# Optimization experiments

Measured on AMD Instinct MI355X. Metric: run time of the kernel, lower is better.

## Reference

```python
import jax, jax.numpy as jnp
import numpy as np

N, C_IN, C_OUT, H = 4096, 1024, 512, 4
D = C_OUT // H  # per-head output dim
TEMP = 1.0


def setup_inputs() -> dict:
    key = jax.random.key(0)
    ks = jax.random.split(key, 6)
    node_feats = jax.random.normal(ks[0], (N, C_IN), dtype=jnp.float32)
    # sparse 0/1 adjacency mask, avg degree ~ 0.02*N
    adj_matrix = jax.random.bernoulli(ks[1], 0.02, (N, N)).astype(jnp.float32)
    lim_w = np.sqrt(6.0 / (C_IN + D))
    lim_v = np.sqrt(6.0 / (D + 1))
    W = jax.random.uniform(ks[2], (H, C_IN, D), jnp.float32, -lim_w, lim_w)
    b = jnp.zeros((H, D), dtype=jnp.float32)
    v0 = jax.random.uniform(ks[3], (H, D), jnp.float32, -lim_v, lim_v)
    v1 = jax.random.uniform(ks[4], (H, D), jnp.float32, -lim_v, lim_v)
    return {"node_feats": node_feats, "adj_matrix": adj_matrix,
            "W": W, "b": b, "v0": v0, "v1": v1}


def reference(node_feats, adj_matrix, W, b, v0, v1):
    # per-head linear projection: [H, N, D]
    h = jnp.einsum('nc,hcd->hnd', node_feats, W) + b[:, None, :]
    f1 = jnp.einsum('hnd,hd->hn', h, v0)  # [H, N]
    f2 = jnp.einsum('hnd,hd->hn', h, v1)  # [H, N]
    logits = adj_matrix[None, :, :] * (f1[:, :, None] + f2[:, None, :])
    # torch to_sparse drops exact zeros; sparse.softmax normalizes over
    # the remaining (nonzero) entries only, zeros stay zero when densified.
    mask = logits != 0
    vals = (jax.nn.sigmoid(logits) - 0.5) / TEMP
    rowmax = jnp.max(jnp.where(mask, vals, -1e30), axis=-1, keepdims=True)
    e = jnp.where(mask, jnp.exp(vals - rowmax), 0.0)
    denom = jnp.sum(e, axis=-1, keepdims=True)
    p = jnp.where(denom > 0, e / jnp.maximum(denom, 1e-30), 0.0)
    out = jnp.einsum('hnm,hmd->hnd', p, h)  # [H, N, D]
    # concat heads along feature dim -> [N, H*D]
    return out.transpose(1, 0, 2).reshape(node_feats.shape[0], -1)
```

## Files before the change

### kernel.cpp

```cpp
#include <hip/hip_runtime.h>
#include <hip/hip_bf16.h>

#define N_NODES 4096
#define C_IN    1024
#define H_HEADS 4
#define D_HEAD  128
#define C_OUT   512
#define DEG_CAP 256

typedef __attribute__((ext_vector_type(8))) short short8;
typedef __attribute__((ext_vector_type(8))) unsigned short u16x8;
typedef __attribute__((ext_vector_type(4))) float f32x4;

__device__ __forceinline__ unsigned short f2bf(float f) {
    unsigned u = __float_as_uint(f);
    u += 0x7FFFu + ((u >> 16) & 1u);
    return (unsigned short)(u >> 16);
}
__device__ __forceinline__ float bf2f(unsigned short u) {
    return __uint_as_float((unsigned)u << 16);
}
__device__ __forceinline__ float sigv(float s) {
    return 1.f / (1.f + __expf(-s)) - 0.5f;
}

#define GLOAD_LDS16(gp, lp)                                                        \
    __builtin_amdgcn_global_load_lds(                                              \
        (const __attribute__((address_space(1))) unsigned int*)(gp),               \
        (__attribute__((address_space(3))) unsigned int*)(lp), 16, 0, 0)

__global__ void k_cvt(const float* __restrict__ X, const float* __restrict__ W,
                      unsigned short* __restrict__ Xb, unsigned short* __restrict__ Wt,
                      float* __restrict__ F12) {
    if (blockIdx.x < 2048) {
        int g = blockIdx.x * blockDim.x + threadIdx.x;
        const float4* s = (const float4*)(X + (size_t)g * 8);
        float4 a = s[0], b = s[1];
        ushort4 p0, p1;
        p0.x = f2bf(a.x); p0.y = f2bf(a.y); p0.z = f2bf(a.z); p0.w = f2bf(a.w);
        p1.x = f2bf(b.x); p1.y = f2bf(b.y); p1.z = f2bf(b.z); p1.w = f2bf(b.w);
        ushort4* d = (ushort4*)(Xb + (size_t)g * 8);
        d[0] = p0; d[1] = p1;
    } else if (blockIdx.x < 2560) {
        int g = (blockIdx.x - 2048) * blockDim.x + threadIdx.x;
        int o = g * 4;
        int c  = o & 1023;
        int hd = o >> 10;
        int d  = hd & 127;
        int h  = hd >> 7;
        const float* src = W + (size_t)h * C_IN * D_HEAD + (size_t)c * D_HEAD + d;
        ushort4 p;
        p.x = f2bf(src[0 * D_HEAD]);
        p.y = f2bf(src[1 * D_HEAD]);
        p.z = f2bf(src[2 * D_HEAD]);
        p.w = f2bf(src[3 * D_HEAD]);
        *(ushort4*)(Wt + o) = p;
    } else {
        int g = (blockIdx.x - 2560) * blockDim.x + threadIdx.x;
        *(f32x4*)(F12 + (size_t)g * 4) = (f32x4){0.f, 0.f, 0.f, 0.f};
    }
}

__global__ void k_work(const unsigned short* __restrict__ Xb,
                       const unsigned short* __restrict__ Wt,
                       const float* __restrict__ bias,
                       const float* __restrict__ v0, const float* __restrict__ v1,
                       const float* __restrict__ adj,
                       unsigned short* __restrict__ Hb,
                       float* __restrict__ F1, float* __restrict__ F2,
                       unsigned short* __restrict__ idx, int* __restrict__ nnz) {
    __shared__ __align__(16) unsigned char smem[32768];
    const int t    = threadIdx.x;
    const int lane = t & 63;
    const int wid  = t >> 6;

    if (blockIdx.x < 512) {
        unsigned short* ldsA = (unsigned short*)smem;
        unsigned short* ldsB = ldsA + 2 * 64 * 64;
        const int wrow = wid >> 1, wcol = wid & 1;
        const int bid  = blockIdx.x;
        const int lin  = (bid & 7) * 64 + (bid >> 3);
        const int rowStart = (lin >> 3) * 64;
        const int colStart = (lin & 7) * 64;

        f32x4 acc[2][2];
#pragma unroll
        for (int m = 0; m < 2; ++m)
#pragma unroll
            for (int n = 0; n < 2; ++n) acc[m][n] = (f32x4){0.f, 0.f, 0.f, 0.f};

        const int lrow = lane >> 2;
        const int lkq  = (lane & 3) ^ ((lane >> 3) & 3);

        auto stage = [&](int buf, int k0) {
#pragma unroll
            for (int ii = 0; ii < 2; ++ii) {
                int c  = wid * 2 + ii;
                int h  = c >> 2, rb = c & 3;
                const unsigned short* g =
                    Xb + (size_t)(rowStart + rb * 16 + lrow) * C_IN + k0 + h * 32 + lkq * 8;
                GLOAD_LDS16(g, ldsA + buf * 4096 + h * 2048 + rb * 512);
            }
#pragma unroll
            for (int ii = 0; ii < 2; ++ii) {
                int c  = wid * 2 + ii;
                int h  = c >> 2, db = c & 3;
                const unsigned short* g =
                    Wt + (size_t)(colStart + db * 16 + lrow) * C_IN + k0 + h * 32 + lkq * 8;
                GLOAD_LDS16(g, ldsB + buf * 4096 + h * 2048 + db * 512);
            }
        };

        stage(0, 0);
        __syncthreads();

        const int fr = lane & 15;
        const int sw = ((lane >> 4) ^ ((fr >> 1) & 3)) * 8;
        int cur = 0;
        for (int kt = 0; kt < 16; ++kt) {
            if (kt < 15) stage(cur ^ 1, (kt + 1) * 64);
            const unsigned short* __restrict__ lA = ldsA + cur * 4096;
            const unsigned short* __restrict__ lB = ldsB + cur * 4096;
#pragma unroll
            for (int h = 0; h < 2; ++h) {
                short8 bfr[2];
#pragma unroll
                for (int n = 0; n < 2; ++n)
                    bfr[n] = *(const short8*)(lB + h * 2048 + (wcol * 32 + n * 16 + fr) * 32 + sw);
#pragma unroll
                for (int m = 0; m < 2; ++m) {
                    short8 a = *(const short8*)(lA + h * 2048 + (wrow * 32 + m * 16 + fr) * 32 + sw);
#pragma unroll
                    for (int n = 0; n < 2; ++n)
                        acc[m][n] = __builtin_amdgcn_mfma_f32_16x16x32_bf16(a, bfr[n], acc[m][n], 0, 0, 0);
                }
            }
            __syncthreads();
            cur ^= 1;
        }

        const int c0 = colStart + wcol * 32 + (lane & 15);
        const int c1 = c0 + 16;
        const int head = c0 >> 7;
        const float bb0 = bias[c0], bb1 = bias[c1];
        const float v0c0 = v0[c0], v0c1 = v0[c1];
        const float v1c0 = v1[c0], v1c1 = v1[c1];
#pragma unroll
        for (int m = 0; m < 2; ++m) {
            int row_g = rowStart + wrow * 32 + m * 16 + (lane >> 4) * 4;
#pragma unroll
            for (int r = 0; r < 4; ++r) {
                float h0 = acc[m][0][r] + bb0;
                float h1 = acc[m][1][r] + bb1;
                Hb[(size_t)(row_g + r) * C_OUT + c0] = f2bf(h0);
                Hb[(size_t)(row_g + r) * C_OUT + c1] = f2bf(h1);
                float p1 = h0 * v0c0 + h1 * v0c1;
                float p2 = h0 * v1c0 + h1 * v1c1;
#pragma unroll
                for (int off = 8; off; off >>= 1) {
                    p1 += __shfl_xor(p1, off);
                    p2 += __shfl_xor(p2, off);
                }
                if ((lane & 15) == 0) {
                    atomicAdd(&F1[(row_g + r) * 4 + head], p1);
                    atomicAdd(&F2[(row_g + r) * 4 + head], p2);
                }
            }
        }
    } else {
        int* wtot = (int*)smem;
        const int i = blockIdx.x - 512;
        const float4* arow = (const float4*)(adj + (size_t)i * N_NODES);
        float4 av[4];
#pragma unroll
        for (int r = 0; r < 4; ++r) av[r] = arow[r * 256 + t];

        int cnt = 0;
#pragma unroll
        for (int r = 0; r < 4; ++r)
            cnt += (av[r].x != 0.f) + (av[r].y != 0.f) + (av[r].z != 0.f) + (av[r].w != 0.f);
        int v = cnt;
#pragma unroll
        for (int off = 1; off < 64; off <<= 1) {
            int u = __shfl_up(v, off);
            if (lane >= off) v += u;
        }
        if (lane == 63) wtot[wid] = v;
        __syncthreads();
        int wpre = 0, total = 0;
#pragma unroll
        for (int w = 0; w < 4; ++w) {
            int tw = wtot[w];
            if (w < wid) wpre += tw;
            total += tw;
        }
        int off = wpre + v - cnt;
        unsigned short* ir = idx + (size_t)i * DEG_CAP;
#pragma unroll
        for (int r = 0; r < 4; ++r) {
            int j0 = (r * 256 + t) * 4;
            if (av[r].x != 0.f) { if (off < DEG_CAP) ir[off] = (unsigned short)j0;       off++; }
            if (av[r].y != 0.f) { if (off < DEG_CAP) ir[off] = (unsigned short)(j0 + 1); off++; }
            if (av[r].z != 0.f) { if (off < DEG_CAP) ir[off] = (unsigned short)(j0 + 2); off++; }
            if (av[r].w != 0.f) { if (off < DEG_CAP) ir[off] = (unsigned short)(j0 + 3); off++; }
        }
        if (t == 0) nnz[i] = min(total, DEG_CAP);
    }
}

__global__ void k_pv(const unsigned short* __restrict__ idx, const int* __restrict__ nnz,
                     const float* __restrict__ F1, const float* __restrict__ F2,
                     const unsigned short* __restrict__ Hb, float* __restrict__ Out) {
    __shared__ unsigned short jl[DEG_CAP];
    __shared__ float ev[H_HEADS][DEG_CAP];

    const int i    = blockIdx.x;
    const int t    = threadIdx.x;
    const int lane = t & 63;
    const int w    = t >> 6;

    const int nv = nnz[i];

    ushort4 jv = *(const ushort4*)(idx + (size_t)i * DEG_CAP + 4 * lane);
    *(ushort4*)(jl + 4 * lane) = jv;

    const float f1h = F1[i * 4 + w];
    float dsum = 0.f;
#pragma unroll
    for (int s = 0; s < 4; ++s) {
        int e = lane + 64 * s;
        float ee = 0.f;
        if (e < nv) {
            int j = jl[e];
            float sg = f1h + F2[j * 4 + w];
            ee = (sg != 0.f) ? __expf(sigv(sg)) : 0.f;
        }
        ev[w][e] = ee;
        dsum += ee;
    }
#pragma unroll
    for (int o2 = 32; o2; o2 >>= 1) dsum += __shfl_xor(dsum, o2);

    const unsigned short* __restrict__ hp = Hb + (size_t)w * D_HEAD + 2 * lane;
    float a0 = 0.f, a1 = 0.f, b0 = 0.f, b1 = 0.f;
    int jj = 0;
#pragma unroll 4
    for (; jj + 1 < nv; jj += 2) {
        int ja = jl[jj], jb = jl[jj + 1];
        float ea = ev[w][jj], eb = ev[w][jj + 1];
        unsigned pa = *(const unsigned*)(hp + (size_t)ja * C_OUT);
        unsigned pb = *(const unsigned*)(hp + (size_t)jb * C_OUT);
        a0 += ea * bf2f((unsigned short)(pa & 0xFFFFu));
        a1 += ea * bf2f((unsigned short)(pa >> 16));
        b0 += eb * bf2f((unsigned short)(pb & 0xFFFFu));
        b1 += eb * bf2f((unsigned short)(pb >> 16));
    }
    if (jj < nv) {
        int ja = jl[jj];
        float ea = ev[w][jj];
        unsigned pa = *(const unsigned*)(hp + (size_t)ja * C_OUT);
        a0 += ea * bf2f((unsigned short)(pa & 0xFFFFu));
        a1 += ea * bf2f((unsigned short)(pa >> 16));
    }

    float2 o;
    if (dsum > 0.f) {
        float inv = 1.f / fmaxf(dsum, 1e-30f);
        o.x = (a0 + b0) * inv;
        o.y = (a1 + b1) * inv;
    } else {
        o.x = 0.f; o.y = 0.f;
    }
    *(float2*)(Out + (size_t)i * C_OUT + w * D_HEAD + 2 * lane) = o;
}

extern "C" void kernel_launch(void* const* d_in, const int* in_sizes, int n_in,
                              void* d_out, int out_size, void* d_ws, size_t ws_size,
                              hipStream_t stream) {
    const float* X   = (const float*)d_in[0];
    const float* adj = (const float*)d_in[1];
    const float* W   = (const float*)d_in[2];
    const float* b   = (const float*)d_in[3];
    const float* v0  = (const float*)d_in[4];
    const float* v1  = (const float*)d_in[5];
    float* out = (float*)d_out;

    char* ws = (char*)d_ws;
    unsigned short* Wt  = (unsigned short*)ws;
    unsigned short* Xb  = (unsigned short*)(ws + (size_t)1 * 1024 * 1024);
    unsigned short* Hb  = (unsigned short*)(ws + (size_t)9 * 1024 * 1024);
    float*          F1  = (float*)(ws + (size_t)13 * 1024 * 1024);
    float*          F2  = F1 + N_NODES * 4;
    unsigned short* idx = (unsigned short*)(ws + (size_t)14 * 1024 * 1024);
    int*            nnz = (int*)(ws + (size_t)16 * 1024 * 1024);

    k_cvt<<<2592, 256, 0, stream>>>(X, W, Xb, Wt, F1);
    k_work<<<512 + N_NODES, 256, 0, stream>>>(Xb, Wt, b, v0, v1, adj, Hb, F1, F2, idx, nnz);
    k_pv<<<N_NODES, 256, 0, stream>>>(idx, nnz, F1, F2, Hb, out);
}
```

Before: 59.70 us.

## Move adjacency compaction into prep kernel, split GEMM out, widen gather loads

Adjacency row compaction now runs in the same launch as the bf16 conversion of X and W, and the GEMM becomes its own kernel with statically sized LDS. Conversion blocks now handle 32 elements of X per thread, and the F1/F2 zeroing is folded into the first 32 blocks. The PV gather now splits each wave into two halves, each lane loading 4 bf16 values per neighbour row, with a cross-half shuffle reduction at the end. The aim is to rebalance work across launches so the large adjacency scan no longer shares a launch with the GEMM, and to issue fewer, wider gather loads, at the cost of half the lanes sitting idle during the final store.

```diff
diff --git a/kernel.cpp b/kernel.cpp
--- a/kernel.cpp
+++ b/kernel.cpp
@@ -10,6 +10,7 @@
 
 typedef __attribute__((ext_vector_type(8))) short short8;
 typedef __attribute__((ext_vector_type(8))) unsigned short u16x8;
+typedef __attribute__((ext_vector_type(4))) unsigned short u16x4;
 typedef __attribute__((ext_vector_type(4))) float f32x4;
 
 __device__ __forceinline__ unsigned short f2bf(float f) {
@@ -29,146 +30,44 @@
         (const __attribute__((address_space(1))) unsigned int*)(gp),               \
         (__attribute__((address_space(3))) unsigned int*)(lp), 16, 0, 0)
 
-__global__ void k_cvt(const float* __restrict__ X, const float* __restrict__ W,
-                      unsigned short* __restrict__ Xb, unsigned short* __restrict__ Wt,
-                      float* __restrict__ F12) {
-    if (blockIdx.x < 2048) {
-        int g = blockIdx.x * blockDim.x + threadIdx.x;
-        const float4* s = (const float4*)(X + (size_t)g * 8);
-        float4 a = s[0], b = s[1];
-        ushort4 p0, p1;
-        p0.x = f2bf(a.x); p0.y = f2bf(a.y); p0.z = f2bf(a.z); p0.w = f2bf(a.w);
-        p1.x = f2bf(b.x); p1.y = f2bf(b.y); p1.z = f2bf(b.z); p1.w = f2bf(b.w);
-        ushort4* d = (ushort4*)(Xb + (size_t)g * 8);
-        d[0] = p0; d[1] = p1;
-    } else if (blockIdx.x < 2560) {
-        int g = (blockIdx.x - 2048) * blockDim.x + threadIdx.x;
-        int o = g * 4;
+__global__ void k_prep(const float* __restrict__ X, const float* __restrict__ W,
+                       const float* __restrict__ adj,
+                       unsigned short* __restrict__ Xb, unsigned short* __restrict__ Wt,
+                       float* __restrict__ F12,
+                       unsigned short* __restrict__ idx, int* __restrict__ nnz) {
+    __shared__ int wtot[4];
+    const int t    = threadIdx.x;
+    const int lane = t & 63;
+    const int wid  = t >> 6;
+
+    if (blockIdx.x < 512) {
+        size_t g = (size_t)blockIdx.x * 256 + t;
+        const float4* s = (const float4*)(X + g * 32);
+        ushort4* d = (ushort4*)(Xb + g * 32);
+#pragma unroll
+        for (int q = 0; q < 8; ++q) {
+            float4 a = s[q];
+            ushort4 p;
+            p.x = f2bf(a.x); p.y = f2bf(a.y); p.z = f2bf(a.z); p.w = f2bf(a.w);
+            d[q] = p;
+        }
+        int o = ((int)blockIdx.x * 256 + t) * 4;
         int c  = o & 1023;
         int hd = o >> 10;
-        int d  = hd & 127;
+        int dd = hd & 127;
         int h  = hd >> 7;
-        const float* src = W + (size_t)h * C_IN * D_HEAD + (size_t)c * D_HEAD + d;
+        const float* src = W + (size_t)h * C_IN * D_HEAD + (size_t)c * D_HEAD + dd;
         ushort4 p;
         p.x = f2bf(src[0 * D_HEAD]);
         p.y = f2bf(src[1 * D_HEAD]);
         p.z = f2bf(src[2 * D_HEAD]);
         p.w = f2bf(src[3 * D_HEAD]);
         *(ushort4*)(Wt + o) = p;
+        if (blockIdx.x < 32) {
+            int z = (int)blockIdx.x * 256 + t;
+            *(f32x4*)(F12 + (size_t)z * 4) = (f32x4){0.f, 0.f, 0.f, 0.f};
+        }
     } else {
-        int g = (blockIdx.x - 2560) * blockDim.x + threadIdx.x;
-        *(f32x4*)(F12 + (size_t)g * 4) = (f32x4){0.f, 0.f, 0.f, 0.f};
-    }
-}
-
-__global__ void k_work(const unsigned short* __restrict__ Xb,
-                       const unsigned short* __restrict__ Wt,
-                       const float* __restrict__ bias,
-                       const float* __restrict__ v0, const float* __restrict__ v1,
-                       const float* __restrict__ adj,
-                       unsigned short* __restrict__ Hb,
-                       float* __restrict__ F1, float* __restrict__ F2,
-                       unsigned short* __restrict__ idx, int* __restrict__ nnz) {
-    __shared__ __align__(16) unsigned char smem[32768];
-    const int t    = threadIdx.x;
-    const int lane = t & 63;
-    const int wid  = t >> 6;
-
-    if (blockIdx.x < 512) {
-        unsigned short* ldsA = (unsigned short*)smem;
-        unsigned short* ldsB = ldsA + 2 * 64 * 64;
-        const int wrow = wid >> 1, wcol = wid & 1;
-        const int bid  = blockIdx.x;
-        const int lin  = (bid & 7) * 64 + (bid >> 3);
-        const int rowStart = (lin >> 3) * 64;
-        const int colStart = (lin & 7) * 64;
-
-        f32x4 acc[2][2];
-#pragma unroll
-        for (int m = 0; m < 2; ++m)
-#pragma unroll
-            for (int n = 0; n < 2; ++n) acc[m][n] = (f32x4){0.f, 0.f, 0.f, 0.f};
-
-        const int lrow = lane >> 2;
-        const int lkq  = (lane & 3) ^ ((lane >> 3) & 3);
-
-        auto stage = [&](int buf, int k0) {
-#pragma unroll
-            for (int ii = 0; ii < 2; ++ii) {
-                int c  = wid * 2 + ii;
-                int h  = c >> 2, rb = c & 3;
-                const unsigned short* g =
-                    Xb + (size_t)(rowStart + rb * 16 + lrow) * C_IN + k0 + h * 32 + lkq * 8;
-                GLOAD_LDS16(g, ldsA + buf * 4096 + h * 2048 + rb * 512);
-            }
-#pragma unroll
-            for (int ii = 0; ii < 2; ++ii) {
-                int c  = wid * 2 + ii;
-                int h  = c >> 2, db = c & 3;
-                const unsigned short* g =
-                    Wt + (size_t)(colStart + db * 16 + lrow) * C_IN + k0 + h * 32 + lkq * 8;
-                GLOAD_LDS16(g, ldsB + buf * 4096 + h * 2048 + db * 512);
-            }
-        };
-
-        stage(0, 0);
-        __syncthreads();
-
-        const int fr = lane & 15;
-        const int sw = ((lane >> 4) ^ ((fr >> 1) & 3)) * 8;
-        int cur = 0;
-        for (int kt = 0; kt < 16; ++kt) {
-            if (kt < 15) stage(cur ^ 1, (kt + 1) * 64);
-            const unsigned short* __restrict__ lA = ldsA + cur * 4096;
-            const unsigned short* __restrict__ lB = ldsB + cur * 4096;
-#pragma unroll
-            for (int h = 0; h < 2; ++h) {
-                short8 bfr[2];
-#pragma unroll
-                for (int n = 0; n < 2; ++n)
-                    bfr[n] = *(const short8*)(lB + h * 2048 + (wcol * 32 + n * 16 + fr) * 32 + sw);
-#pragma unroll
-                for (int m = 0; m < 2; ++m) {
-                    short8 a = *(const short8*)(lA + h * 2048 + (wrow * 32 + m * 16 + fr) * 32 + sw);
-#pragma unroll
-                    for (int n = 0; n < 2; ++n)
-                        acc[m][n] = __builtin_amdgcn_mfma_f32_16x16x32_bf16(a, bfr[n], acc[m][n], 0, 0, 0);
-                }
-            }
-            __syncthreads();
-            cur ^= 1;
-        }
-
-        const int c0 = colStart + wcol * 32 + (lane & 15);
-        const int c1 = c0 + 16;
-        const int head = c0 >> 7;
-        const float bb0 = bias[c0], bb1 = bias[c1];
-        const float v0c0 = v0[c0], v0c1 = v0[c1];
-        const float v1c0 = v1[c0], v1c1 = v1[c1];
-#pragma unroll
-        for (int m = 0; m < 2; ++m) {
-            int row_g = rowStart + wrow * 32 + m * 16 + (lane >> 4) * 4;
-#pragma unroll
-            for (int r = 0; r < 4; ++r) {
-                float h0 = acc[m][0][r] + bb0;
-                float h1 = acc[m][1][r] + bb1;
-                Hb[(size_t)(row_g + r) * C_OUT + c0] = f2bf(h0);
-                Hb[(size_t)(row_g + r) * C_OUT + c1] = f2bf(h1);
-                float p1 = h0 * v0c0 + h1 * v0c1;
-                float p2 = h0 * v1c0 + h1 * v1c1;
-#pragma unroll
-                for (int off = 8; off; off >>= 1) {
-                    p1 += __shfl_xor(p1, off);
-                    p2 += __shfl_xor(p2, off);
-                }
-                if ((lane & 15) == 0) {
-                    atomicAdd(&F1[(row_g + r) * 4 + head], p1);
-                    atomicAdd(&F2[(row_g + r) * 4 + head], p2);
-                }
-            }
-        }
-    } else {
-        int* wtot = (int*)smem;
         const int i = blockIdx.x - 512;
         const float4* arow = (const float4*)(adj + (size_t)i * N_NODES);
         float4 av[4];
@@ -205,6 +104,109 @@
             if (av[r].w != 0.f) { if (off < DEG_CAP) ir[off] = (unsigned short)(j0 + 3); off++; }
         }
         if (t == 0) nnz[i] = min(total, DEG_CAP);
+    }
+}
+
+__global__ void k_gemm(const unsigned short* __restrict__ Xb,
+                       const unsigned short* __restrict__ Wt,
+                       const float* __restrict__ bias,
+                       const float* __restrict__ v0, const float* __restrict__ v1,
+                       unsigned short* __restrict__ Hb,
+                       float* __restrict__ F1, float* __restrict__ F2) {
+    __shared__ __align__(16) unsigned short ldsA[2 * 64 * 64];
+    __shared__ __align__(16) unsigned short ldsB[2 * 64 * 64];
+    const int t    = threadIdx.x;
+    const int lane = t & 63;
+    const int wid  = t >> 6;
+    const int wrow = wid >> 1, wcol = wid & 1;
+    const int bid  = blockIdx.x;
+    const int lin  = (bid & 7) * 64 + (bid >> 3);
+    const int rowStart = (lin >> 3) * 64;
+    const int colStart = (lin & 7) * 64;
+
+    f32x4 acc[2][2];
+#pragma unroll
+    for (int m = 0; m < 2; ++m)
+#pragma unroll
+        for (int n = 0; n < 2; ++n) acc[m][n] = (f32x4){0.f, 0.f, 0.f, 0.f};
+
+    const int lrow = lane >> 2;
+    const int lkq  = (lane & 3) ^ ((lane >> 3) & 3);
+
+    auto stage = [&](int buf, int k0) {
+#pragma unroll
+        for (int ii = 0; ii < 2; ++ii) {
+            int c  = wid * 2 + ii;
+            int h  = c >> 2, rb = c & 3;
+            const unsigned short* g =
+                Xb + (size_t)(rowStart + rb * 16 + lrow) * C_IN + k0 + h * 32 + lkq * 8;
+            GLOAD_LDS16(g, ldsA + buf * 4096 + h * 2048 + rb * 512);
+        }
+#pragma unroll
+        for (int ii = 0; ii < 2; ++ii) {
+            int c  = wid * 2 + ii;
+            int h  = c >> 2, db = c & 3;
+            const unsigned short* g =
+                Wt + (size_t)(colStart + db * 16 + lrow) * C_IN + k0 + h * 32 + lkq * 8;
+            GLOAD_LDS16(g, ldsB + buf * 4096 + h * 2048 + db * 512);
+        }
+    };
+
+    stage(0, 0);
+    __syncthreads();
+
+    const int fr = lane & 15;
+    const int sw = ((lane >> 4) ^ ((fr >> 1) & 3)) * 8;
+    int cur = 0;
+    for (int kt = 0; kt < 16; ++kt) {
+        if (kt < 15) stage(cur ^ 1, (kt + 1) * 64);
+        const unsigned short* __restrict__ lA = ldsA + cur * 4096;
+        const unsigned short* __restrict__ lB = ldsB + cur * 4096;
+#pragma unroll
+        for (int h = 0; h < 2; ++h) {
+            short8 bfr[2];
+#pragma unroll
+            for (int n = 0; n < 2; ++n)
+                bfr[n] = *(const short8*)(lB + h * 2048 + (wcol * 32 + n * 16 + fr) * 32 + sw);
+#pragma unroll
+            for (int m = 0; m < 2; ++m) {
+                short8 a = *(const short8*)(lA + h * 2048 + (wrow * 32 + m * 16 + fr) * 32 + sw);
+#pragma unroll
+                for (int n = 0; n < 2; ++n)
+                    acc[m][n] = __builtin_amdgcn_mfma_f32_16x16x32_bf16(a, bfr[n], acc[m][n], 0, 0, 0);
+            }
+        }
+        __syncthreads();
+        cur ^= 1;
+    }
+
+    const int c0 = colStart + wcol * 32 + (lane & 15);
+    const int c1 = c0 + 16;
+    const int head = c0 >> 7;
+    const float bb0 = bias[c0], bb1 = bias[c1];
+    const float v0c0 = v0[c0], v0c1 = v0[c1];
+    const float v1c0 = v1[c0], v1c1 = v1[c1];
+#pragma unroll
+    for (int m = 0; m < 2; ++m) {
+        int row_g = rowStart + wrow * 32 + m * 16 + (lane >> 4) * 4;
+#pragma unroll
+        for (int r = 0; r < 4; ++r) {
+            float h0 = acc[m][0][r] + bb0;
+            float h1 = acc[m][1][r] + bb1;
+            Hb[(size_t)(row_g + r) * C_OUT + c0] = f2bf(h0);
+            Hb[(size_t)(row_g + r) * C_OUT + c1] = f2bf(h1);
+            float p1 = h0 * v0c0 + h1 * v0c1;
+            float p2 = h0 * v1c0 + h1 * v1c1;
+#pragma unroll
+            for (int off = 8; off; off >>= 1) {
+                p1 += __shfl_xor(p1, off);
+                p2 += __shfl_xor(p2, off);
+            }
+            if ((lane & 15) == 0) {
+                atomicAdd(&F1[(row_g + r) * 4 + head], p1);
+                atomicAdd(&F2[(row_g + r) * 4 + head], p2);
+            }
+        }
     }
 }
 
@@ -241,37 +243,46 @@
 #pragma unroll
     for (int o2 = 32; o2; o2 >>= 1) dsum += __shfl_xor(dsum, o2);
 
-    const unsigned short* __restrict__ hp = Hb + (size_t)w * D_HEAD + 2 * lane;
-    float a0 = 0.f, a1 = 0.f, b0 = 0.f, b1 = 0.f;
-    int jj = 0;
+    const int half = lane >> 5;
+    const int sub  = lane & 31;
+    const unsigned short* __restrict__ hp = Hb + (size_t)w * D_HEAD + sub * 4;
+    f32x4 accA = {0.f, 0.f, 0.f, 0.f}, accB = {0.f, 0.f, 0.f, 0.f};
+    int jj = half;
 #pragma unroll 4
-    for (; jj + 1 < nv; jj += 2) {
-        int ja = jl[jj], jb = jl[jj + 1];
-        float ea = ev[w][jj], eb = ev[w][jj + 1];
-        unsigned pa = *(const unsigned*)(hp + (size_t)ja * C_OUT);
-        unsigned pb = *(const unsigned*)(hp + (size_t)jb * C_OUT);
-        a0 += ea * bf2f((unsigned short)(pa & 0xFFFFu));
-        a1 += ea * bf2f((unsigned short)(pa >> 16));
-        b0 += eb * bf2f((unsigned short)(pb & 0xFFFFu));
-        b1 += eb * bf2f((unsigned short)(pb >> 16));
+    for (; jj + 2 < nv; jj += 4) {
+        int ja = jl[jj], jb = jl[jj + 2];
+        float ea = ev[w][jj], eb = ev[w][jj + 2];
+        u16x4 ha = *(const u16x4*)(hp + (size_t)ja * C_OUT);
+        u16x4 hb = *(const u16x4*)(hp + (size_t)jb * C_OUT);
+#pragma unroll
+        for (int k = 0; k < 4; ++k) accA[k] += ea * bf2f(ha[k]);
+#pragma unroll
+        for (int k = 0; k < 4; ++k) accB[k] += eb * bf2f(hb[k]);
     }
     if (jj < nv) {
         int ja = jl[jj];
         float ea = ev[w][jj];
-        unsigned pa = *(const unsigned*)(hp + (size_t)ja * C_OUT);
-        a0 += ea * bf2f((unsigned short)(pa & 0xFFFFu));
-        a1 += ea * bf2f((unsigned short)(pa >> 16));
-    }
-
-    float2 o;
-    if (dsum > 0.f) {
-        float inv = 1.f / fmaxf(dsum, 1e-30f);
-        o.x = (a0 + b0) * inv;
-        o.y = (a1 + b1) * inv;
-    } else {
-        o.x = 0.f; o.y = 0.f;
-    }
-    *(float2*)(Out + (size_t)i * C_OUT + w * D_HEAD + 2 * lane) = o;
+        u16x4 ha = *(const u16x4*)(hp + (size_t)ja * C_OUT);
+#pragma unroll
+        for (int k = 0; k < 4; ++k) accA[k] += ea * bf2f(ha[k]);
+    }
+#pragma unroll
+    for (int k = 0; k < 4; ++k) {
+        accA[k] += accB[k];
+        accA[k] += __shfl_xor(accA[k], 32);
+    }
+
+    if (half == 0) {
+        float4 o;
+        if (dsum > 0.f) {
+            float inv = 1.f / fmaxf(dsum, 1e-30f);
+            o.x = accA[0] * inv; o.y = accA[1] * inv;
+            o.z = accA[2] * inv; o.w = accA[3] * inv;
+        } else {
+            o.x = o.y = o.z = o.w = 0.f;
+        }
+        *(float4*)(Out + (size_t)i * C_OUT + w * D_HEAD + sub * 4) = o;
+    }
 }
 
 extern "C" void kernel_launch(void* const* d_in, const int* in_sizes, int n_in,
@@ -294,7 +305,7 @@
     unsigned short* idx = (unsigned short*)(ws + (size_t)14 * 1024 * 1024);
     int*            nnz = (int*)(ws + (size_t)16 * 1024 * 1024);
 
-    k_cvt<<<2592, 256, 0, stream>>>(X, W, Xb, Wt, F1);
-    k_work<<<512 + N_NODES, 256, 0, stream>>>(Xb, Wt, b, v0, v1, adj, Hb, F1, F2, idx, nnz);
+    k_prep<<<512 + N_NODES, 256, 0, stream>>>(X, W, adj, Xb, Wt, F1, idx, nnz);
+    k_gemm<<<512, 256, 0, stream>>>(Xb, Wt, b, v0, v1, Hb, F1, F2);
     k_pv<<<N_NODES, 256, 0, stream>>>(idx, nnz, F1, F2, Hb, out);
 }
```

Result: slower. 72.98 us (+22.3%).
